# Optimization experiments

Measured on AMD Instinct MI355X. Metric: run time of the kernel, lower is better.

The kernel has to match this reference:

```python
import jax, jax.numpy as jnp
import numpy as np

B, H, S = 128, 256, 19
K0, D0 = 512, 32
K1, D1 = 512, 64
K2, D2 = 512, 64


def _conv(x, w, b):
    # 3x3 SAME conv, NCHW / OIHW
    y = jax.lax.conv_general_dilated(x, w, (1, 1), 'SAME',
                                     dimension_numbers=('NCHW', 'OIHW', 'NCHW'))
    return y + b[None, :, None, None]


def _bn(x, g, b, eps=1e-5):
    # BatchNorm2d in training mode: batch statistics over (N, H, W)
    m = x.mean((0, 2, 3), keepdims=True)
    v = x.var((0, 2, 3), keepdims=True)
    return g[None, :, None, None] * (x - m) * jax.lax.rsqrt(v + eps) + b[None, :, None, None]


def _vq(lat, E):
    # cdist^2 -> argmin -> gather, with straight-through gradient copy
    shp = lat.shape
    d = E.shape[1]
    lp = lat.reshape(-1, d)                                   # row-major flatten, as torch .view
    dist = (lp * lp).sum(-1, keepdims=True) + (E * E).sum(-1) - 2.0 * (lp @ E.T)
    k = jnp.argmin(dist, axis=-1)
    zd = E[k]
    zg = lp + jax.lax.stop_gradient(zd - lp)
    return k.reshape(shp[0], -1), zd.reshape(shp), zg.reshape(shp)


def setup_inputs() -> dict:
    key = jax.random.key(0)
    ks = iter(jax.random.split(key, 64))
    def rn(shape, s=0.02):
        return (s * jax.random.normal(next(ks), shape)).astype(jnp.float32)
    inp = {
        'observations': jax.random.normal(next(ks), (B, 18, S, S), jnp.float32),
        'hierarchy_usages': jax.random.uniform(next(ks), (B, 2), jnp.float32),
        'h0_conv_w': rn((H, 18, 3, 3), 0.05), 'h0_conv_b': jnp.zeros((H,)),
        'h0_bn_g': jnp.ones((H,)), 'h0_bn_b': jnp.zeros((H,)),
        'rb_c1_w': rn((3, H, H, 3, 3)), 'rb_c1_b': jnp.zeros((3, H)),
        'rb_bn1_g': jnp.ones((3, H)), 'rb_bn1_b': jnp.zeros((3, H)),
        'rb_c2_w': rn((3, H, H, 3, 3)), 'rb_c2_b': jnp.zeros((3, H)),
        'rb_bn2_g': jnp.ones((3, H)), 'rb_bn2_b': jnp.zeros((3, H)),
        'h0_conv2_w': rn((32, H, 3, 3)), 'h0_conv2_b': jnp.zeros((32,)),
        'h0_bn2_g': jnp.ones((32,)), 'h0_bn2_b': jnp.zeros((32,)),
        'E0': rn((K0, D0)), 'E1': rn((K1, D1)), 'E2': rn((K2, D2)),
        'h1_fc_w': rn((D0 * S * S, 256)), 'h1_fc_b': jnp.zeros((256,)),
        'h1_fc2_w': rn((256, D1 * 8)), 'h1_fc2_b': jnp.zeros((D1 * 8,)),
        'h2_fc_w': rn((D1 * 8, 128)), 'h2_fc_b': jnp.zeros((128,)),
        'h2_fc2_w': rn((128, D2 * 8)), 'h2_fc2_b': jnp.zeros((D2 * 8,)),
        'h2_fc3_w': rn((D2 * 8, 128)), 'h2_fc3_b': jnp.zeros((128,)),
        'h2_fc4_w': rn((128, D1 * 8)), 'h2_fc4_b': jnp.zeros((D1 * 8,)),
        'h1_fc3_w': rn((D1 * 8, 256)), 'h1_fc3_b': jnp.zeros((256,)),
        'h1_fc4_w': rn((256, D0 * S * S)), 'h1_fc4_b': jnp.zeros((D0 * S * S,)),
        'policy_w': rn((32 * S * S, 362)), 'policy_b': jnp.zeros((362,)),
        'value_w': rn((32 * S * S, 1)), 'value_b': jnp.zeros((1,)),
    }
    return inp


def _forward(observations, hierarchy_usages, h0_conv_w, h0_conv_b, h0_bn_g, h0_bn_b,
             rb_c1_w, rb_c1_b, rb_bn1_g, rb_bn1_b, rb_c2_w, rb_c2_b, rb_bn2_g, rb_bn2_b,
             h0_conv2_w, h0_conv2_b, h0_bn2_g, h0_bn2_b, E0, E1, E2,
             h1_fc_w, h1_fc_b, h1_fc2_w, h1_fc2_b, h2_fc_w, h2_fc_b, h2_fc2_w, h2_fc2_b,
             h2_fc3_w, h2_fc3_b, h2_fc4_w, h2_fc4_b, h1_fc3_w, h1_fc3_b, h1_fc4_w, h1_fc4_b,
             policy_w, policy_b, value_w, value_b):
    n = observations.shape[0]
    x = jax.nn.relu(_bn(_conv(observations, h0_conv_w, h0_conv_b), h0_bn_g, h0_bn_b))
    for i in range(3):
        xi = x
        x = jax.nn.relu(_bn(_conv(x, rb_c1_w[i], rb_c1_b[i]), rb_bn1_g[i], rb_bn1_b[i]))
        x = _bn(_conv(x, rb_c2_w[i], rb_c2_b[i]), rb_bn2_g[i], rb_bn2_b[i])
        x = jax.nn.relu(xi + x)
    x = jnp.tanh(_bn(_conv(x, h0_conv2_w, h0_conv2_b), h0_bn2_g, h0_bn2_b))  # [B,32,19,19]
    ze0 = x
    k0, zq0, zql0 = _vq(x, E0)
    em0 = jnp.broadcast_to(E0.mean(0)[None, :, None, None], (n, E0.shape[1], S, S))
    x = jax.lax.stop_gradient(x).reshape(-1, 32 * S * S)
    x = jax.nn.relu(x @ h1_fc_w + h1_fc_b)
    x = jnp.tanh(x @ h1_fc2_w + h1_fc2_b).reshape(-1, E1.shape[1], 8)
    ze1 = x
    k1, zq1, zql1 = _vq(x, E1)
    em1 = jnp.broadcast_to(E1.mean(0)[None, :, None], (n, E1.shape[1], 8))
    x = jax.lax.stop_gradient(x).reshape(-1, E1.shape[1] * 8)
    x = jax.nn.relu(x @ h2_fc_w + h2_fc_b)
    x = jnp.tanh(x @ h2_fc2_w + h2_fc2_b).reshape(-1, E2.shape[1], 8)
    ze2 = x
    k2, zq2, zql2 = _vq(x, E2)
    em2 = jnp.broadcast_to(E2.mean(0)[None, :, None], (n, E2.shape[1], 8))
    # top-down decoder path
    x = zql2.reshape(-1, E2.shape[1] * 8)
    x = jax.nn.relu(x @ h2_fc3_w + h2_fc3_b)
    x = jnp.tanh(x @ h2_fc4_w + h2_fc4_b).reshape(-1, E1.shape[1], 8)
    u1 = hierarchy_usages[:, 1][:, None, None]
    x = u1 * zql1 + (1.0 - u1) * x
    x = x.reshape(-1, E1.shape[1] * 8)
    x = jax.nn.relu(x @ h1_fc3_w + h1_fc3_b)
    x = jnp.tanh(x @ h1_fc4_w + h1_fc4_b).reshape(-1, E0.shape[1], S, S)
    u0 = hierarchy_usages[:, 0][:, None, None, None]
    x = u0 * zql0 + (1.0 - u0) * x
    x = x.reshape(-1, 32 * S * S)
    policy = x @ policy_w + policy_b
    value = jnp.tanh(x @ value_w + value_b)
    return (policy, value, ze0, ze1, ze2, zq0, zq1, zq2, k0, k1, k2,
            zql0, zql1, zql2, em0, em1, em2)


def reference(observations, hierarchy_usages, h0_conv_w, h0_conv_b, h0_bn_g, h0_bn_b,
              rb_c1_w, rb_c1_b, rb_bn1_g, rb_bn1_b, rb_c2_w, rb_c2_b, rb_bn2_g, rb_bn2_b,
              h0_conv2_w, h0_conv2_b, h0_bn2_g, h0_bn2_b, E0, E1, E2,
              h1_fc_w, h1_fc_b, h1_fc2_w, h1_fc2_b, h2_fc_w, h2_fc_b, h2_fc2_w, h2_fc2_b,
              h2_fc3_w, h2_fc3_b, h2_fc4_w, h2_fc4_b, h1_fc3_w, h1_fc3_b, h1_fc4_w, h1_fc4_b,
              policy_w, policy_b, value_w, value_b):
    return _forward(observations, hierarchy_usages, h0_conv_w, h0_conv_b, h0_bn_g, h0_bn_b,
                    rb_c1_w, rb_c1_b, rb_bn1_g, rb_bn1_b, rb_c2_w, rb_c2_b, rb_bn2_g, rb_bn2_b,
                    h0_conv2_w, h0_conv2_b, h0_bn2_g, h0_bn2_b, E0, E1, E2,
                    h1_fc_w, h1_fc_b, h1_fc2_w, h1_fc2_b, h2_fc_w, h2_fc_b, h2_fc2_w, h2_fc2_b,
                    h2_fc3_w, h2_fc3_b, h2_fc4_w, h2_fc4_b, h1_fc3_w, h1_fc3_b, h1_fc4_w, h1_fc4_b,
                    policy_w, policy_b, value_w, value_b)
```

## Files before the change

kernel.cpp:

```cpp
#include <hip/hip_runtime.h>
#include <hip/hip_bf16.h>

typedef long long i64;
typedef __attribute__((ext_vector_type(8))) short bf16x8;
typedef __attribute__((ext_vector_type(4))) float f32x4;

static constexpr i64 OUT_POLICY = 0;
static constexpr i64 OUT_VALUE  = 46336;
static constexpr i64 OUT_ZE0    = 46464;
static constexpr i64 OUT_ZE1    = 1525120;
static constexpr i64 OUT_ZE2    = 1590656;
static constexpr i64 OUT_ZQ0    = 1656192;
static constexpr i64 OUT_ZQ1    = 3134848;
static constexpr i64 OUT_ZQ2    = 3200384;
static constexpr i64 OUT_K0     = 3265920;
static constexpr i64 OUT_K1     = 3312128;
static constexpr i64 OUT_K2     = 3313152;
static constexpr i64 OUT_ZQL0   = 3314176;
static constexpr i64 OUT_ZQL1   = 4792832;
static constexpr i64 OUT_ZQL2   = 4858368;
static constexpr i64 OUT_EM0    = 4923904;
static constexpr i64 OUT_EM1    = 6402560;
static constexpr i64 OUT_EM2    = 6468096;
static constexpr i64 OUT_TOTAL  = 6533632;
// ... 11 lines not shown
}

__global__ void wtr_k(const float* __restrict__ w, float* __restrict__ wt,
                      int COUT, int CIN)
{
    int total = COUT * CIN * 9;
    for (int idx = blockIdx.x * blockDim.x + threadIdx.x; idx < total;
         idx += gridDim.x * blockDim.x) {
        int co = idx / (CIN * 9);
        int r  = idx - co * CIN * 9;
        int ci = r / 9;
        int tap = r - ci * 9;
        wt[((i64)tap * CIN + ci) * COUT + co] = w[idx];
    }
}

__global__ void wtr4_k(const float* __restrict__ w, short* __restrict__ wt4,
                       int CIN, int COUT)
{
    int NC = CIN / 32;
    int total = NC * 9 * 2 * 8192;
    for (int idx = blockIdx.x * blockDim.x + threadIdx.x; idx < total;
         idx += gridDim.x * blockDim.x) {
        int tile = idx >> 13;
        int pos  = idx & 8191;
        int row   = pos >> 6;
        int sslot = (pos >> 3) & 7;
        int r     = pos & 7;
        int slot  = sslot ^ (row & 7);
        int k2    = slot * 8 + r;
        int ct = tile & 1;
        int s  = tile >> 1;
        int c  = s / 9, t = s - c * 9;
        int co = ct * 128 + row;
        int ci = c * 32 + (k2 & 31);
        short outv = 0;
        if (co < COUT) {
            float v = w[((i64)co * CIN + ci) * 9 + t];
            float hf;
            short hs = bf16_hi(v, &hf);
            outv = (k2 < 32) ? hs : bf16_of(v - hf);
        }
        wt4[idx] = outv;
    }
}

template<int CIN>
__global__ __launch_bounds__(256)
void convmfma_k(const float* __restrict__ X, const short* __restrict__ WT4,
                float* __restrict__ Y, int coutT)
{
    constexpr int NC = CIN / 32;
    constexpr int NS = NC * 9;
    __shared__ short At[2][8192];
    __shared__ short Bt[2][8192];
    const int tid  = threadIdx.x;
    const int lane = tid & 63;
    const int w    = tid >> 6;
    const int wco  = (w & 1) * 64;
    const int wsp  = (w >> 1) * 64;
    const int col0 = blockIdx.x * 128;
    const int ct   = blockIdx.y;
    const int co0  = ct * 128;

    const int spS = tid & 127;
    const int cig = tid >> 7;
    const int colS = col0 + spS;
    const int nS = colS / 361;
    const int sS = colS - nS * 361;
    const int yS = sS / 19, xS = sS - yS * 19;
    const float* Xb = X + (i64)nS * CIN * 361 + sS;

    float xv[16];

#define A_ISSUE(BUF, S)                                                         \
    {                                                                           \
        const short* gp0 = WT4 + ((i64)((S) * 2 + ct) << 13) + (w << 11) + (lane << 3); \
        short* lp0 = &At[BUF][(w << 11)];                                       \
        __builtin_amdgcn_global_load_lds(gp0,        lp0,        16, 0, 0);     \
        __builtin_amdgcn_global_load_lds(gp0 + 512,  lp0 + 512,  16, 0, 0);     \
        __builtin_amdgcn_global_load_lds(gp0 + 1024, lp0 + 1024, 16, 0, 0);     \
        __builtin_amdgcn_global_load_lds(gp0 + 1536, lp0 + 1536, 16, 0, 0);     \
    }

#define B_LOAD(S)                                                               \
    {                                                                           \
        const int c_ = (S) / 9, t_ = (S) - c_ * 9;                              \
        const int ky_ = t_ / 3, kx_ = t_ - ky_ * 3;                             \
        const bool v_ = (yS + ky_ >= 1) & (yS + ky_ <= 19) &                    \
                        (xS + kx_ >= 1) & (xS + kx_ <= 19);                     \
        const float* xp_ = Xb + (i64)(c_ * 32 + cig * 16) * 361                 \
                              + (ky_ - 1) * 19 + (kx_ - 1);                     \
        _Pragma("unroll")                                                       \
        for (int j = 0; j < 16; j++) xv[j] = v_ ? xp_[(i64)j * 361] : 0.f;      \
    }

#define B_WRITE(BUF)                                                            \
    {                                                                           \
        bf16x8 h0, h1, l0, l1;                                                  \
        _Pragma("unroll")                                                       \
        for (int j = 0; j < 8; j++) {                                           \
            float hf;                                                           \
            short hs = bf16_hi(xv[j], &hf);                                     \
            h0[j] = hs; l0[j] = bf16_of(xv[j] - hf);                            \
        }                                                                       \
        _Pragma("unroll")                                                       \
        for (int j = 0; j < 8; j++) {                                           \
            float hf;                                                           \
            short hs = bf16_hi(xv[8 + j], &hf);                                 \
            h1[j] = hs; l1[j] = bf16_of(xv[8 + j] - hf);                        \
        }                                                                       \
        short* bp = &Bt[BUF][spS << 6];                                         \
        const int sw = spS & 7;                                                 \
        *(bf16x8*)(bp + (((cig * 2 + 0) ^ sw) << 3)) = h0;                      \
        *(bf16x8*)(bp + (((cig * 2 + 1) ^ sw) << 3)) = h1;                      \
        *(bf16x8*)(bp + (((4 + cig * 2 + 0) ^ sw) << 3)) = l0;                  \
        *(bf16x8*)(bp + (((4 + cig * 2 + 1) ^ sw) << 3)) = l1;                  \
    }

    f32x4 acc[4][4];
#pragma unroll
    for (int i = 0; i < 4; i++)
#pragma unroll
        for (int j = 0; j < 4; j++) acc[i][j] = (f32x4){0.f, 0.f, 0.f, 0.f};

    A_ISSUE(0, 0)
    B_LOAD(0)
    B_WRITE(0)
    int cur = 0;
    for (int s = 0; s < NS; s++) {
        __syncthreads();
        if (s + 1 < NS) { A_ISSUE(cur ^ 1, s + 1) B_LOAD(s + 1) }
        {
            bf16x8 bfr[2][4];
#pragma unroll
            for (int hb = 0; hb < 2; hb++)
#pragma unroll
                for (int fb = 0; fb < 4; fb++) {
                    int row = wsp + fb * 16 + (lane & 15);
                    int slot = hb * 4 + (lane >> 4);
                    bfr[hb][fb] = *(const bf16x8*)&Bt[cur][(row << 6) + (((slot ^ (row & 7))) << 3)];
                }
#pragma unroll
            for (int ha = 0; ha < 2; ha++)
#pragma unroll
                for (int fa = 0; fa < 4; fa++) {
                    int row = wco + fa * 16 + (lane & 15);
                    int slot = ha * 4 + (lane >> 4);
                    bf16x8 af = *(const bf16x8*)&At[cur][(row << 6) + (((slot ^ (row & 7))) << 3)];
#pragma unroll
                    for (int hb = 0; hb < 2; hb++)
#pragma unroll
                        for (int fb = 0; fb < 4; fb++)
                            acc[fa][fb] = __builtin_amdgcn_mfma_f32_16x16x32_bf16(
                                af, bfr[hb][fb], acc[fa][fb], 0, 0, 0);
                }
        }
        if (s + 1 < NS) B_WRITE(cur ^ 1)
        cur ^= 1;
    }
#undef A_ISSUE
#undef B_LOAD
#undef B_WRITE

#pragma unroll
    for (int fb = 0; fb < 4; fb++) {
        int col = col0 + wsp + fb * 16 + (lane & 15);
        int nT = col / 361, sT = col - nT * 361;
        float* yp = Y + ((i64)nT * coutT + co0 + wco) * 361 + sT;
#pragma unroll
        for (int fa = 0; fa < 4; fa++)
#pragma unroll
            for (int r = 0; r < 4; r++) {
                int m = fa * 16 + (lane >> 4) * 4 + r;
                if (co0 + wco + m < coutT) yp[(i64)m * 361] = acc[fa][fb][r];
            }
    }
}

template<int CIN>
__global__ __launch_bounds__(256)
void convgemm_k(const float* __restrict__ X, const float* __restrict__ wt,
                float* __restrict__ Y, int wtW, int coW0, int coutT)
{
    constexpr int NCB = (CIN + 15) / 16;
    constexpr int NS  = 9 * NCB;
    __shared__ float Ws[2][16][128];
    __shared__ float Bs[2][16][128];
    const int tid  = threadIdx.x;
    const int col0 = blockIdx.x * 128;
    const int co0  = blockIdx.y * 128;
    const int tn = tid & 15;
    const int tm = (tid >> 4) & 15;
    const int kkS  = tid >> 5;
    const int cS0  = (tid & 31) * 4;

    int y_[4], x_[4];
    const float* Xb[4];
#pragma unroll
    for (int j = 0; j < 4; j++) {
        int colj = col0 + cS0 + j;
        int nj = colj / 361;
        int sj = colj - nj * 361;
        y_[j] = sj / 19;
        x_[j] = sj - y_[j] * 19;
        Xb[j] = X + ((i64)nj * CIN) * 361 + sj;
    }

    float4 wA, wB, bA, bB;

#define STAGE(S)                                                               \
    {                                                                          \
        const int tap_ = (S) / NCB, cb_ = ((S) % NCB) * 16;                    \
        const int ky_ = tap_ / 3, kx_ = tap_ - ky_ * 3;                        \
        const int doff_ = (ky_ - 1) * 19 + (kx_ - 1);                          \
        const int ci0_ = cb_ + kkS, ci1_ = ci0_ + 8;                           \
// ... 53 lines not shown
                    acc[wi][bj] = fmaf(wv[wi], bv[bj], acc[wi][bj]);
        }
        if (s + 1 < NS) WRITE(cur ^ 1)
        cur ^= 1;
    }
#undef STAGE
#undef WRITE

#pragma unroll
    for (int bj = 0; bj < 8; bj++) {
        int lc = (bj < 4) ? (tn * 4 + bj) : (64 + tn * 4 + bj - 4);
        int colT = col0 + lc;
        int nT = colT / 361;
        int sT = colT - nT * 361;
        float* yp = Y + ((i64)nT * coutT + co0) * 361 + sT;
#pragma unroll
        for (int wi = 0; wi < 8; wi++) {
            int co = (wi < 4) ? (tm * 4 + wi) : (64 + tm * 4 + wi - 4);
            if (co0 + co < coutT) yp[(i64)co * 361] = acc[wi][bj];
        }
    }
}

__global__ __launch_bounds__(256)
void bnstats_k(const float* __restrict__ x, const float* __restrict__ g,
               const float* __restrict__ b, float* __restrict__ scale,
               float* __restrict__ shift, int C)
{
    const int c = blockIdx.x;
    float s = 0.f, s2 = 0.f;
    for (int n = 0; n < 128; n++) {
        const float* p = x + ((i64)n * C + c) * 361;
        for (int i = threadIdx.x; i < 361; i += 256) {
            float v = p[i]; s += v; s2 += v * v;
        }
    }
    __shared__ float rs[4], rq[4];
    for (int o = 32; o > 0; o >>= 1) { s += __shfl_down(s, o); s2 += __shfl_down(s2, o); }
    int lane = threadIdx.x & 63, wid = threadIdx.x >> 6;
    if (lane == 0) { rs[wid] = s; rq[wid] = s2; }
    __syncthreads();
    if (threadIdx.x == 0) {
        float S = rs[0] + rs[1] + rs[2] + rs[3];
        float Q = rq[0] + rq[1] + rq[2] + rq[3];
        const float inv = 1.f / 46208.f;
        float m  = S * inv;
        float var = Q * inv - m * m;
        float sc = g[c] * rsqrtf(var + 1e-5f);
        scale[c] = sc;
        shift[c] = b[c] - m * sc;
    }
}

__global__ void bn_relu_k(float* __restrict__ x, const float* __restrict__ scale,
                          const float* __restrict__ shift, int C, int total)
{
    for (int i = blockIdx.x * blockDim.x + threadIdx.x; i < total; i += gridDim.x * blockDim.x) {
        int c = (i / 361) % C;
        float v = fmaf(x[i], scale[c], shift[c]);
        x[i] = v > 0.f ? v : 0.f;
    }
}

__global__ void bn_add_relu_full_k(float* __restrict__ xa, const float* __restrict__ xc,
                                   const float* __restrict__ scale, const float* __restrict__ shift,
                                   int C, int total)
{
    for (int i = blockIdx.x * blockDim.x + threadIdx.x; i < total; i += gridDim.x * blockDim.x) {
        int c = (i / 361) % C;
        float v = xa[i] + fmaf(xc[i], scale[c], shift[c]);
        xa[i] = v > 0.f ? v : 0.f;
    }
}

__global__ void bn_add_relu_slice_k(float* __restrict__ xa, const float* __restrict__ xc,
                                    const float* __restrict__ scale, const float* __restrict__ shift,
                                    int cbase, int total)
{
    for (int i = blockIdx.x * blockDim.x + threadIdx.x; i < total; i += gridDim.x * blockDim.x) {
        int s = i % 361;
        int t = i / 361;
        int ch = t % 64;
        int n = t / 64;
        i64 ai = ((i64)n * 256 + cbase + ch) * 361 + s;
        float v = xa[ai] + fmaf(xc[i], scale[ch], shift[ch]);
        xa[ai] = v > 0.f ? v : 0.f;
    }
}

__global__ void bn_tanh_ws_k(const float* __restrict__ x, const float* __restrict__ scale,
                             const float* __restrict__ shift, float* __restrict__ zf, int total)
{
    for (int i = blockIdx.x * blockDim.x + threadIdx.x; i < total; i += gridDim.x * blockDim.x) {
        int c = (i / 361) & 31;
        zf[i] = tanhf(fmaf(x[i], scale[c], shift[c]));
    }
}

__global__ void prep_k(const float* __restrict__ E0, const float* __restrict__ E1,
                       const float* __restrict__ E2,
                       float* __restrict__ ee0, float* __restrict__ ee1, float* __restrict__ ee2,
                       float* __restrict__ cm0, float* __restrict__ cm1, float* __restrict__ cm2)
{
    int t = threadIdx.x;
    if (blockIdx.x == 0) {
        float s = 0.f; const float* e = E0 + (i64)t * 32;
        for (int d = 0; d < 32; d++) s += e[d] * e[d];
        ee0[t] = s;
    } else if (blockIdx.x == 1) {
        float s = 0.f; const float* e = E1 + (i64)t * 64;
        for (int d = 0; d < 64; d++) s += e[d] * e[d];
        ee1[t] = s;
    } else if (blockIdx.x == 2) {
        float s = 0.f; const float* e = E2 + (i64)t * 64;
        for (int d = 0; d < 64; d++) s += e[d] * e[d];
        ee2[t] = s;
    } else {
        if (t < 32) {
            float s = 0.f; for (int k = 0; k < 512; k++) s += E0[k * 32 + t];
            cm0[t] = s * (1.f / 512.f);
        } else if (t >= 64 && t < 128) {
            int d = t - 64; float s = 0.f; for (int k = 0; k < 512; k++) s += E1[k * 64 + d];
            cm1[d] = s * (1.f / 512.f);
        } else if (t >= 128 && t < 192) {
            int d = t - 128; float s = 0.f; for (int k = 0; k < 512; k++) s += E2[k * 64 + d];
            cm2[d] = s * (1.f / 512.f);
        }
    }
}

__global__ __launch_bounds__(256)
void vq0_k(const float* __restrict__ z, const float* __restrict__ E,
           const float* __restrict__ ee, float* __restrict__ zqf, int* __restrict__ ki)
{
    __shared__ float Es[256 * 32];
    int row = blockIdx.x * 256 + threadIdx.x;
    const bool live = row < 46208;
    const float* zp = z + (i64)(live ? row : 0) * 32;
    float zv[32]; float zz = 0.f;
// ... 100 lines not shown
        int m = tm * 8 + i;
#pragma unroll
        for (int j = 0; j < 4; j++) {
            int n = n0 + tn * 4 + j;
            if (n < N) part[((i64)ks * 128 + m) * N + n] = acc[i][j];
        }
    }
}

__global__ void combine_k(const float* __restrict__ part, const float* __restrict__ bias,
                          float* __restrict__ of, int MN, int N, int ksplit, int act)
{
    for (int i = blockIdx.x * blockDim.x + threadIdx.x; i < MN; i += gridDim.x * blockDim.x) {
        float s = 0.f;
        for (int t = 0; t < ksplit; t++) s += part[(i64)t * MN + i];
        s += bias[i % N];
        if (act == 1) s = s > 0.f ? s : 0.f;
        else if (act == 2) s = tanhf(s);
        of[i] = s;
    }
}

__global__ void blend_k(const float* __restrict__ q, const float* __restrict__ d,
                        const float* __restrict__ hu, int col, float* __restrict__ o,
                        int per_b, int total)
{
    for (int i = blockIdx.x * blockDim.x + threadIdx.x; i < total; i += gridDim.x * blockDim.x) {
        float u = hu[(i / per_b) * 2 + col];
        o[i] = u * q[i] + (1.f - u) * d[i];
    }
}

__global__ __launch_bounds__(256)
void value_k(const float* __restrict__ x, const float* __restrict__ w,
             const float* __restrict__ b, float* __restrict__ valf)
{
    int m = blockIdx.x;
    float s = 0.f;
    const float* xp = x + (i64)m * 11552;
    for (int k = threadIdx.x; k < 11552; k += 256) s = fmaf(xp[k], w[k], s);
    for (int o = 32; o > 0; o >>= 1) s += __shfl_down(s, o);
    __shared__ float r[4];
    int lane = threadIdx.x & 63, wid = threadIdx.x >> 6;
    if (lane == 0) r[wid] = s;
    __syncthreads();
    if (threadIdx.x == 0)
        valf[m] = tanhf(r[0] + r[1] + r[2] + r[3] + b[0]);
}

__global__ void emit_f32_k(const float* __restrict__ src, float* __restrict__ out, i64 off, int n)
{
    for (int i = blockIdx.x * blockDim.x + threadIdx.x; i < n; i += gridDim.x * blockDim.x)
        out[off + i] = src[i];
}

__global__ void emit_k_k(const int* __restrict__ ki, float* __restrict__ out, i64 off, int n)
{
    for (int i = blockIdx.x * blockDim.x + threadIdx.x; i < n; i += gridDim.x * blockDim.x)
        out[off + i] = (float)ki[i];
}

__global__ void emit_em_k(const float* __restrict__ cm, float* __restrict__ out, i64 off,
                          int D, int SPL, int total)
{
    for (int i = blockIdx.x * blockDim.x + threadIdx.x; i < total; i += gridDim.x * blockDim.x) {
        int c = (i / SPL) % D;
        out[off + i] = cm[c];
    }
}

__global__ void marker_k(float* __restrict__ out, int code)
{
    if (threadIdx.x < 64) out[threadIdx.x] = 3000.f + 100.f * code;
}

__global__ void sentinel_k(float* __restrict__ out)
{
    if (threadIdx.x < 128) out[OUT_VALUE + threadIdx.x] = 2000.0f;
}

extern "C" void kernel_launch(void* const* d_in, const int* in_sizes, int n_in,
                              void* d_out, int out_size, void* d_ws, size_t ws_size,
                              hipStream_t stream)
{
    float* out = (float*)d_out;

    int bad = -1;
    if (out_size != (int)OUT_TOTAL) bad = 0;
    else if (n_in != 41) bad = 1;
    else if (in_sizes[0] != 128 * 18 * 361) bad = 2;
    else if (in_sizes[21] != 11552 * 256) bad = 3;
    if (bad >= 0) { marker_k<<<1, 64, 0, stream>>>(out, bad); return; }

    const float* obs   = (const float*)d_in[0];
    const float* hier  = (const float*)d_in[1];
    const float* c0w   = (const float*)d_in[2];
    const float* bn0g  = (const float*)d_in[4];
    const float* bn0b  = (const float*)d_in[5];
    const float* rb1w  = (const float*)d_in[6];
    const float* rbn1g = (const float*)d_in[8];
    const float* rbn1b = (const float*)d_in[9];
    const float* rb2w  = (const float*)d_in[10];
    const float* rbn2g = (const float*)d_in[12];
    const float* rbn2b = (const float*)d_in[13];
    const float* c2w   = (const float*)d_in[14];
    const float* bn2g  = (const float*)d_in[16];
// ... 12 lines not shown
    const float* polw  = (const float*)d_in[37]; const float* polb  = (const float*)d_in[38];
    const float* valw  = (const float*)d_in[39]; const float* valb  = (const float*)d_in[40];

    float* wsf = (float*)d_ws;

    const size_t NEED_A = (size_t)36732928 * 4;
    const size_t NEED_C = (size_t)27860992 * 4;
    if (ws_size < NEED_C) {
        sentinel_k<<<1, 128, 0, stream>>>(out);
        return;
    }
    const bool fullC = (ws_size >= NEED_A);

    float* scale = wsf + 0;        float* shift = wsf + 256;
    float* ee0 = wsf + 512;        float* ee1 = wsf + 1024;   float* ee2 = wsf + 1536;
    float* cm0 = wsf + 2048;       float* cm1 = wsf + 2112;   float* cm2 = wsf + 2176;
    int*   k0i = (int*)(wsf + 4096);
    int*   k1i = (int*)(wsf + 50304);
    int*   k2i = (int*)(wsf + 51328);
    float* h1a  = wsf + 53248;
    float* ze1f = wsf + 86016;
    float* zq1f = wsf + 151552;
    float* h2a  = wsf + 217088;
    float* ze2f = wsf + 233472;
    float* zq2f = wsf + 299008;
    float* h2b  = wsf + 364544;
    float* decf = wsf + 380928;
    float* x1f  = wsf + 446464;
    float* h1b  = wsf + 512000;
    float* polf = wsf + 544768;
    float* valf = wsf + 591104;

    float* A    = wsf + 655360;
    float* B    = wsf + 12484608;
    float* C    = wsf + 24313856;
    float* WT   = fullC ? (wsf + 36143104) : (wsf + 27271168);
    float* ze0f = A;
    float* zq0f = wsf + 655360 + 1572864;
    float* dec0 = wsf + 655360 + 3145728;
    float* xf   = wsf + 655360 + 4718592;
    float* part = B;

    short* WT4 = (short*)d_out;

    const int TOT256 = 128 * 256 * 361;
    const int TOT32  = 128 * 32 * 361;
    const int TOT64  = 128 * 64 * 361;

    prep_k<<<4, 512, 0, stream>>>(E0, E1, E2, ee0, ee1, ee2, cm0, cm1, cm2);

    wtr_k<<<64, 256, 0, stream>>>(c0w, WT, 256, 18);
    convgemm_k<18><<<dim3(361, 2), 256, 0, stream>>>(obs, WT, A, 256, 0, 256);
    bnstats_k<<<256, 256, 0, stream>>>(A, bn0g, bn0b, scale, shift, 256);
    bn_relu_k<<<1024, 256, 0, stream>>>(A, scale, shift, 256, TOT256);

    for (int i = 0; i < 3; i++) {
        if (fullC) {
            wtr4_k<<<1024, 256, 0, stream>>>(rb1w + (i64)i * 589824, WT4, 256, 256);
            convmfma_k<256><<<dim3(361, 2), 256, 0, stream>>>(A, WT4, B, 256);
        } else {
            wtr_k<<<576, 256, 0, stream>>>(rb1w + (i64)i * 589824, WT, 256, 256);
            convgemm_k<256><<<dim3(361, 2), 256, 0, stream>>>(A, WT, B, 256, 0, 256);
        }
        bnstats_k<<<256, 256, 0, stream>>>(B, rbn1g + i * 256, rbn1b + i * 256, scale, shift, 256);
        bn_relu_k<<<1024, 256, 0, stream>>>(B, scale, shift, 256, TOT256);
        if (fullC) {
            wtr4_k<<<1024, 256, 0, stream>>>(rb2w + (i64)i * 589824, WT4, 256, 256);
            convmfma_k<256><<<dim3(361, 2), 256, 0, stream>>>(B, WT4, C, 256);
            bnstats_k<<<256, 256, 0, stream>>>(C, rbn2g + i * 256, rbn2b + i * 256, scale, shift, 256);
            bn_add_relu_full_k<<<1024, 256, 0, stream>>>(A, C, scale, shift, 256, TOT256);
        } else {
            wtr_k<<<576, 256, 0, stream>>>(rb2w + (i64)i * 589824, WT, 256, 256);
            for (int c = 0; c < 4; c++) {
                convgemm_k<256><<<dim3(361, 1), 256, 0, stream>>>(B, WT, C, 256, c * 64, 64);
                bnstats_k<<<64, 256, 0, stream>>>(C, rbn2g + i * 256 + c * 64,
                                                  rbn2b + i * 256 + c * 64, scale, shift, 64);
                bn_add_relu_slice_k<<<1024, 256, 0, stream>>>(A, C, scale, shift, c * 64, TOT64);
            }
        }
    }

    if (fullC) {
        wtr4_k<<<1024, 256, 0, stream>>>(c2w, WT4, 256, 32);
        convmfma_k<256><<<dim3(361, 1), 256, 0, stream>>>(A, WT4, C, 32);
    } else {
        wtr_k<<<72, 256, 0, stream>>>(c2w, WT, 32, 256);
        convgemm_k<256><<<dim3(361, 1), 256, 0, stream>>>(A, WT, C, 32, 0, 32);
    }
    bnstats_k<<<32, 256, 0, stream>>>(C, bn2g, bn2b, scale, shift, 32);
    bn_tanh_ws_k<<<1024, 256, 0, stream>>>(C, scale, shift, ze0f, TOT32);

    vq0_k<<<181, 256, 0, stream>>>(ze0f, E0, ee0, zq0f, k0i);

    gemm_part_k<<<dim3(4, 32), 256, 0, stream>>>(ze0f, fc1w, part, 11552, 256, 361);
    combine_k<<<128, 256, 0, stream>>>(part, fc1b, h1a, 128 * 256, 256, 32, 1);
    gemm_part_k<<<dim3(8, 4), 256, 0, stream>>>(h1a, fc2w, part, 256, 512, 64);
    combine_k<<<256, 256, 0, stream>>>(part, fc2b, ze1f, 128 * 512, 512, 4, 2);
    vq64_k<<<4, 256, 0, stream>>>(ze1f, E1, ee1, zq1f, k1i);

    gemm_part_k<<<dim3(2, 8), 256, 0, stream>>>(ze1f, h2fw, part, 512, 128, 64);
    combine_k<<<64, 256, 0, stream>>>(part, h2fb, h2a, 128 * 128, 128, 8, 1);
    gemm_part_k<<<dim3(8, 2), 256, 0, stream>>>(h2a, h2f2w, part, 128, 512, 64);
    combine_k<<<256, 256, 0, stream>>>(part, h2f2b, ze2f, 128 * 512, 512, 2, 2);
    vq64_k<<<4, 256, 0, stream>>>(ze2f, E2, ee2, zq2f, k2i);

    gemm_part_k<<<dim3(2, 8), 256, 0, stream>>>(zq2f, h2f3w, part, 512, 128, 64);
    combine_k<<<64, 256, 0, stream>>>(part, h2f3b, h2b, 128 * 128, 128, 8, 1);
    gemm_part_k<<<dim3(8, 2), 256, 0, stream>>>(h2b, h2f4w, part, 128, 512, 64);
    combine_k<<<256, 256, 0, stream>>>(part, h2f4b, decf, 128 * 512, 512, 2, 2);
    blend_k<<<256, 256, 0, stream>>>(zq1f, decf, hier, 1, x1f, 512, 65536);

    gemm_part_k<<<dim3(4, 8), 256, 0, stream>>>(x1f, h1f3w, part, 512, 256, 64);
    combine_k<<<128, 256, 0, stream>>>(part, h1f3b, h1b, 128 * 256, 256, 8, 1);
    gemm_part_k<<<dim3(181, 2), 256, 0, stream>>>(h1b, h1f4w, part, 256, 11552, 128);
    combine_k<<<1024, 256, 0, stream>>>(part, h1f4b, dec0, TOT32, 11552, 2, 2);
    blend_k<<<1024, 256, 0, stream>>>(zq0f, dec0, hier, 0, xf, 11552, TOT32);

    gemm_part_k<<<dim3(6, 16), 256, 0, stream>>>(xf, polw, part, 11552, 362, 722);
    combine_k<<<256, 256, 0, stream>>>(part, polb, polf, 128 * 362, 362, 16, 0);
    value_k<<<128, 256, 0, stream>>>(xf, valw, valb, valf);

    emit_f32_k<<<128, 256, 0, stream>>>(polf, out, OUT_POLICY, 46336);
    emit_f32_k<<<1, 128, 0, stream>>>(valf, out, OUT_VALUE, 128);
    emit_f32_k<<<1024, 256, 0, stream>>>(ze0f, out, OUT_ZE0, TOT32);
    emit_f32_k<<<256, 256, 0, stream>>>(ze1f, out, OUT_ZE1, 65536);
    emit_f32_k<<<256, 256, 0, stream>>>(ze2f, out, OUT_ZE2, 65536);
    emit_f32_k<<<1024, 256, 0, stream>>>(zq0f, out, OUT_ZQ0, TOT32);
    emit_f32_k<<<256, 256, 0, stream>>>(zq1f, out, OUT_ZQ1, 65536);
    emit_f32_k<<<256, 256, 0, stream>>>(zq2f, out, OUT_ZQ2, 65536);
    emit_k_k<<<181, 256, 0, stream>>>(k0i, out, OUT_K0, 46208);
    emit_k_k<<<4, 256, 0, stream>>>(k1i, out, OUT_K1, 1024);
    emit_k_k<<<4, 256, 0, stream>>>(k2i, out, OUT_K2, 1024);
    emit_f32_k<<<1024, 256, 0, stream>>>(zq0f, out, OUT_ZQL0, TOT32);
    emit_f32_k<<<256, 256, 0, stream>>>(zq1f, out, OUT_ZQL1, 65536);
    emit_f32_k<<<256, 256, 0, stream>>>(zq2f, out, OUT_ZQL2, 65536);
    emit_em_k<<<1024, 256, 0, stream>>>(cm0, out, OUT_EM0, 32, 361, TOT32);
    emit_em_k<<<256, 256, 0, stream>>>(cm1, out, OUT_EM1, 64, 8, 65536);
    emit_em_k<<<256, 256, 0, stream>>>(cm2, out, OUT_EM2, 64, 8, 65536);
}
```

Baseline: 3.365 ms.

## Deepen conv MFMA pipeline, vectorize BN kernels, merge fallback conv, fuse emits

The MFMA conv main loop now prefetches the activation registers two stages ahead using two register sets, and replaces __syncthreads with hand-written waitcnt plus barrier that leaves outstanding vector loads in flight. This aims to hide global load latency behind the MFMA work. The BN+ReLU and BN+add+ReLU elementwise kernels switch to float4 accesses, and the non-fullC fallback runs a single full conv instead of four 64-channel slices. The duplicated zq/zql output copies are merged into one kernel that writes both. The manual vmcnt(16) count depends on how many loads the compiler actually issues and is fragile, and the extra register set adds register pressure.

```diff
diff --git a/kernel.cpp b/kernel.cpp
--- a/kernel.cpp
+++ b/kernel.cpp
@@ -106,7 +106,10 @@
     const int yS = sS / 19, xS = sS - yS * 19;
     const float* Xb = X + (i64)nS * CIN * 361 + sS;
 
-    float xv[16];
+    float xvP[16], xvQ[16];
+
+#define BAR16 asm volatile("s_waitcnt vmcnt(16) lgkmcnt(0)\n\ts_barrier" ::: "memory")
+#define BAR0  asm volatile("s_waitcnt vmcnt(0) lgkmcnt(0)\n\ts_barrier" ::: "memory")
 
 #define A_ISSUE(BUF, S)                                                         \
     {                                                                           \
@@ -118,7 +121,7 @@
         __builtin_amdgcn_global_load_lds(gp0 + 1536, lp0 + 1536, 16, 0, 0);     \
     }
 
-#define B_LOAD(S)                                                               \
+#define B_LOAD(S, XV)                                                           \
     {                                                                           \
         const int c_ = (S) / 9, t_ = (S) - c_ * 9;                              \
         const int ky_ = t_ / 3, kx_ = t_ - ky_ * 3;                             \
@@ -127,23 +130,23 @@
         const float* xp_ = Xb + (i64)(c_ * 32 + cig * 16) * 361                 \
                               + (ky_ - 1) * 19 + (kx_ - 1);                     \
         _Pragma("unroll")                                                       \
-        for (int j = 0; j < 16; j++) xv[j] = v_ ? xp_[(i64)j * 361] : 0.f;      \
-    }
-
-#define B_WRITE(BUF)                                                            \
+        for (int j = 0; j < 16; j++) XV[j] = v_ ? xp_[(i64)j * 361] : 0.f;      \
+    }
+
+#define B_WRITE(BUF, XV)                                                        \
     {                                                                           \
         bf16x8 h0, h1, l0, l1;                                                  \
         _Pragma("unroll")                                                       \
         for (int j = 0; j < 8; j++) {                                           \
             float hf;                                                           \
-            short hs = bf16_hi(xv[j], &hf);                                     \
-            h0[j] = hs; l0[j] = bf16_of(xv[j] - hf);                            \
+            short hs = bf16_hi(XV[j], &hf);                                     \
+            h0[j] = hs; l0[j] = bf16_of(XV[j] - hf);                            \
         }                                                                       \
         _Pragma("unroll")                                                       \
         for (int j = 0; j < 8; j++) {                                           \
             float hf;                                                           \
-            short hs = bf16_hi(xv[8 + j], &hf);                                 \
-            h1[j] = hs; l1[j] = bf16_of(xv[8 + j] - hf);                        \
+            short hs = bf16_hi(XV[8 + j], &hf);                                 \
+            h1[j] = hs; l1[j] = bf16_of(XV[8 + j] - hf);                        \
         }                                                                       \
         short* bp = &Bt[BUF][spS << 6];                                         \
         const int sw = spS & 7;                                                 \
@@ -153,50 +156,65 @@
         *(bf16x8*)(bp + (((4 + cig * 2 + 1) ^ sw) << 3)) = l1;                  \
     }
 
+#define COMPUTE(CUR)                                                            \
+    {                                                                           \
+        bf16x8 bfr[2][4];                                                       \
+        _Pragma("unroll")                                                       \
+        for (int hb = 0; hb < 2; hb++)                                          \
+            _Pragma("unroll")                                                   \
+            for (int fb = 0; fb < 4; fb++) {                                    \
+                int row = wsp + fb * 16 + (lane & 15);                          \
+                int slot = hb * 4 + (lane >> 4);                                \
+                bfr[hb][fb] = *(const bf16x8*)&Bt[CUR][(row << 6) + (((slot ^ (row & 7))) << 3)]; \
+            }                                                                   \
+        _Pragma("unroll")                                                       \
+        for (int ha = 0; ha < 2; ha++)                                          \
+            _Pragma("unroll")                                                   \
+            for (int fa = 0; fa < 4; fa++) {                                    \
+                int row = wco + fa * 16 + (lane & 15);                          \
+                int slot = ha * 4 + (lane >> 4);                                \
+                bf16x8 af = *(const bf16x8*)&At[CUR][(row << 6) + (((slot ^ (row & 7))) << 3)]; \
+                _Pragma("unroll")                                               \
+                for (int hb = 0; hb < 2; hb++)                                  \
+                    _Pragma("unroll")                                           \
+                    for (int fb = 0; fb < 4; fb++)                              \
+                        acc[fa][fb] = __builtin_amdgcn_mfma_f32_16x16x32_bf16(  \
+                            af, bfr[hb][fb], acc[fa][fb], 0, 0, 0);             \
+            }                                                                   \
+    }
+
+#define ITER(S, XP, XN)                                                         \
+    {                                                                           \
+        if ((S) + 1 < NS) { BAR16; } else { BAR0; }                             \
+        const int cur_ = ((S) & 1);                                             \
+        if ((S) + 1 < NS) A_ISSUE(cur_ ^ 1, (S) + 1)                            \
+        if ((S) + 2 < NS) B_LOAD((S) + 2, XN)                                   \
+        COMPUTE(cur_)                                                           \
+        if ((S) + 1 < NS) B_WRITE(cur_ ^ 1, XP)                                 \
+    }
+
     f32x4 acc[4][4];
 #pragma unroll
     for (int i = 0; i < 4; i++)
 #pragma unroll
         for (int j = 0; j < 4; j++) acc[i][j] = (f32x4){0.f, 0.f, 0.f, 0.f};
 
+    B_LOAD(0, xvP)
+    B_WRITE(0, xvP)
     A_ISSUE(0, 0)
-    B_LOAD(0)
-    B_WRITE(0)
-    int cur = 0;
-    for (int s = 0; s < NS; s++) {
-        __syncthreads();
-        if (s + 1 < NS) { A_ISSUE(cur ^ 1, s + 1) B_LOAD(s + 1) }
-        {
-            bf16x8 bfr[2][4];
-#pragma unroll
-            for (int hb = 0; hb < 2; hb++)
-#pragma unroll
-                for (int fb = 0; fb < 4; fb++) {
-                    int row = wsp + fb * 16 + (lane & 15);
-                    int slot = hb * 4 + (lane >> 4);
-                    bfr[hb][fb] = *(const bf16x8*)&Bt[cur][(row << 6) + (((slot ^ (row & 7))) << 3)];
-                }
-#pragma unroll
-            for (int ha = 0; ha < 2; ha++)
-#pragma unroll
-                for (int fa = 0; fa < 4; fa++) {
-                    int row = wco + fa * 16 + (lane & 15);
-                    int slot = ha * 4 + (lane >> 4);
-                    bf16x8 af = *(const bf16x8*)&At[cur][(row << 6) + (((slot ^ (row & 7))) << 3)];
-#pragma unroll
-                    for (int hb = 0; hb < 2; hb++)
-#pragma unroll
-                        for (int fb = 0; fb < 4; fb++)
-                            acc[fa][fb] = __builtin_amdgcn_mfma_f32_16x16x32_bf16(
-                                af, bfr[hb][fb], acc[fa][fb], 0, 0, 0);
-                }
-        }
-        if (s + 1 < NS) B_WRITE(cur ^ 1)
-        cur ^= 1;
-    }
+    B_LOAD(1, xvP)
+
+    for (int s = 0; s < NS; s += 2) {
+        ITER(s, xvP, xvQ)
+        ITER(s + 1, xvQ, xvP)
+    }
+#undef BAR16
+#undef BAR0
 #undef A_ISSUE
 #undef B_LOAD
 #undef B_WRITE
+#undef COMPUTE
+#undef ITER
 
 #pragma unroll
     for (int fb = 0; fb < 4; fb++) {
@@ -356,39 +374,36 @@
     }
 }
 
-__global__ void bn_relu_k(float* __restrict__ x, const float* __restrict__ scale,
-                          const float* __restrict__ shift, int C, int total)
-{
-    for (int i = blockIdx.x * blockDim.x + threadIdx.x; i < total; i += gridDim.x * blockDim.x) {
-        int c = (i / 361) % C;
-        float v = fmaf(x[i], scale[c], shift[c]);
-        x[i] = v > 0.f ? v : 0.f;
-    }
-}
-
-__global__ void bn_add_relu_full_k(float* __restrict__ xa, const float* __restrict__ xc,
-                                   const float* __restrict__ scale, const float* __restrict__ shift,
-                                   int C, int total)
-{
-    for (int i = blockIdx.x * blockDim.x + threadIdx.x; i < total; i += gridDim.x * blockDim.x) {
-        int c = (i / 361) % C;
-        float v = xa[i] + fmaf(xc[i], scale[c], shift[c]);
-        xa[i] = v > 0.f ? v : 0.f;
-    }
-}
-
-__global__ void bn_add_relu_slice_k(float* __restrict__ xa, const float* __restrict__ xc,
-                                    const float* __restrict__ scale, const float* __restrict__ shift,
-                                    int cbase, int total)
-{
-    for (int i = blockIdx.x * blockDim.x + threadIdx.x; i < total; i += gridDim.x * blockDim.x) {
-        int s = i % 361;
-        int t = i / 361;
-        int ch = t % 64;
-        int n = t / 64;
-        i64 ai = ((i64)n * 256 + cbase + ch) * 361 + s;
-        float v = xa[ai] + fmaf(xc[i], scale[ch], shift[ch]);
-        xa[ai] = v > 0.f ? v : 0.f;
+__global__ void bn_relu4_k(float4* __restrict__ x, const float* __restrict__ scale,
+                           const float* __restrict__ shift, int C, int total4)
+{
+    for (int i = blockIdx.x * blockDim.x + threadIdx.x; i < total4; i += gridDim.x * blockDim.x) {
+        float4 v = x[i];
+        int e = i * 4;
+        int c0 = (e / 361) % C, c1 = ((e + 1) / 361) % C;
+        int c2 = ((e + 2) / 361) % C, c3 = ((e + 3) / 361) % C;
+        v.x = fmaf(v.x, scale[c0], shift[c0]); v.x = v.x > 0.f ? v.x : 0.f;
+        v.y = fmaf(v.y, scale[c1], shift[c1]); v.y = v.y > 0.f ? v.y : 0.f;
+        v.z = fmaf(v.z, scale[c2], shift[c2]); v.z = v.z > 0.f ? v.z : 0.f;
+        v.w = fmaf(v.w, scale[c3], shift[c3]); v.w = v.w > 0.f ? v.w : 0.f;
+        x[i] = v;
+    }
+}
+
+__global__ void bn_add_relu4_k(float4* __restrict__ xa, const float4* __restrict__ xc,
+                               const float* __restrict__ scale, const float* __restrict__ shift,
+                               int C, int total4)
+{
+    for (int i = blockIdx.x * blockDim.x + threadIdx.x; i < total4; i += gridDim.x * blockDim.x) {
+        float4 a = xa[i], c = xc[i];
+        int e = i * 4;
+        int c0 = (e / 361) % C, c1 = ((e + 1) / 361) % C;
+        int c2 = ((e + 2) / 361) % C, c3 = ((e + 3) / 361) % C;
+        a.x += fmaf(c.x, scale[c0], shift[c0]); a.x = a.x > 0.f ? a.x : 0.f;
+        a.y += fmaf(c.y, scale[c1], shift[c1]); a.y = a.y > 0.f ? a.y : 0.f;
+        a.z += fmaf(c.z, scale[c2], shift[c2]); a.z = a.z > 0.f ? a.z : 0.f;
+        a.w += fmaf(c.w, scale[c3], shift[c3]); a.w = a.w > 0.f ? a.w : 0.f;
+        xa[i] = a;
     }
 }
 
@@ -595,6 +610,16 @@
 {
     for (int i = blockIdx.x * blockDim.x + threadIdx.x; i < n; i += gridDim.x * blockDim.x)
         out[off + i] = src[i];
+}
+
+__global__ void emit_dup_k(const float* __restrict__ src, float* __restrict__ out,
+                           i64 off1, i64 off2, int n)
+{
+    for (int i = blockIdx.x * blockDim.x + threadIdx.x; i < n; i += gridDim.x * blockDim.x) {
+        float v = src[i];
+        out[off1 + i] = v;
+        out[off2 + i] = v;
+    }
 }
 
 __global__ void emit_k_k(const int* __restrict__ ki, float* __restrict__ out, i64 off, int n)
@@ -713,7 +738,7 @@
     wtr_k<<<64, 256, 0, stream>>>(c0w, WT, 256, 18);
     convgemm_k<18><<<dim3(361, 2), 256, 0, stream>>>(obs, WT, A, 256, 0, 256);
     bnstats_k<<<256, 256, 0, stream>>>(A, bn0g, bn0b, scale, shift, 256);
-    bn_relu_k<<<1024, 256, 0, stream>>>(A, scale, shift, 256, TOT256);
+    bn_relu4_k<<<1024, 256, 0, stream>>>((float4*)A, scale, shift, 256, TOT256 / 4);
 
     for (int i = 0; i < 3; i++) {
         if (fullC) {
@@ -724,20 +749,17 @@
             convgemm_k<256><<<dim3(361, 2), 256, 0, stream>>>(A, WT, B, 256, 0, 256);
         }
         bnstats_k<<<256, 256, 0, stream>>>(B, rbn1g + i * 256, rbn1b + i * 256, scale, shift, 256);
-        bn_relu_k<<<1024, 256, 0, stream>>>(B, scale, shift, 256, TOT256);
+        bn_relu4_k<<<1024, 256, 0, stream>>>((float4*)B, scale, shift, 256, TOT256 / 4);
         if (fullC) {
             wtr4_k<<<1024, 256, 0, stream>>>(rb2w + (i64)i * 589824, WT4, 256, 256);
             convmfma_k<256><<<dim3(361, 2), 256, 0, stream>>>(B, WT4, C, 256);
             bnstats_k<<<256, 256, 0, stream>>>(C, rbn2g + i * 256, rbn2b + i * 256, scale, shift, 256);
-            bn_add_relu_full_k<<<1024, 256, 0, stream>>>(A, C, scale, shift, 256, TOT256);
+            bn_add_relu4_k<<<1024, 256, 0, stream>>>((float4*)A, (const float4*)C, scale, shift, 256, TOT256 / 4);
         } else {
             wtr_k<<<576, 256, 0, stream>>>(rb2w + (i64)i * 589824, WT, 256, 256);
-            for (int c = 0; c < 4; c++) {
-                convgemm_k<256><<<dim3(361, 1), 256, 0, stream>>>(B, WT, C, 256, c * 64, 64);
-                bnstats_k<<<64, 256, 0, stream>>>(C, rbn2g + i * 256 + c * 64,
-                                                  rbn2b + i * 256 + c * 64, scale, shift, 64);
-                bn_add_relu_slice_k<<<1024, 256, 0, stream>>>(A, C, scale, shift, c * 64, TOT64);
-            }
+            convgemm_k<256><<<dim3(361, 2), 256, 0, stream>>>(B, WT, C, 256, 0, 256);
+            bnstats_k<<<256, 256, 0, stream>>>(C, rbn2g + i * 256, rbn2b + i * 256, scale, shift, 256);
+            bn_add_relu4_k<<<1024, 256, 0, stream>>>((float4*)A, (const float4*)C, scale, shift, 256, TOT256 / 4);
         }
     }
 
@@ -786,15 +808,12 @@
     emit_f32_k<<<1024, 256, 0, stream>>>(ze0f, out, OUT_ZE0, TOT32);
     emit_f32_k<<<256, 256, 0, stream>>>(ze1f, out, OUT_ZE1, 65536);
     emit_f32_k<<<256, 256, 0, stream>>>(ze2f, out, OUT_ZE2, 65536);
-    emit_f32_k<<<1024, 256, 0, stream>>>(zq0f, out, OUT_ZQ0, TOT32);
-    emit_f32_k<<<256, 256, 0, stream>>>(zq1f, out, OUT_ZQ1, 65536);
-    emit_f32_k<<<256, 256, 0, stream>>>(zq2f, out, OUT_ZQ2, 65536);
+    emit_dup_k<<<1024, 256, 0, stream>>>(zq0f, out, OUT_ZQ0, OUT_ZQL0, TOT32);
+    emit_dup_k<<<256, 256, 0, stream>>>(zq1f, out, OUT_ZQ1, OUT_ZQL1, 65536);
+    emit_dup_k<<<256, 256, 0, stream>>>(zq2f, out, OUT_ZQ2, OUT_ZQL2, 65536);
     emit_k_k<<<181, 256, 0, stream>>>(k0i, out, OUT_K0, 46208);
     emit_k_k<<<4, 256, 0, stream>>>(k1i, out, OUT_K1, 1024);
     emit_k_k<<<4, 256, 0, stream>>>(k2i, out, OUT_K2, 1024);
-    emit_f32_k<<<1024, 256, 0, stream>>>(zq0f, out, OUT_ZQL0, TOT32);
-    emit_f32_k<<<256, 256, 0, stream>>>(zq1f, out, OUT_ZQL1, 65536);
-    emit_f32_k<<<256, 256, 0, stream>>>(zq2f, out, OUT_ZQL2, 65536);
     emit_em_k<<<1024, 256, 0, stream>>>(cm0, out, OUT_EM0, 32, 361, TOT32);
     emit_em_k<<<256, 256, 0, stream>>>(cm1, out, OUT_EM1, 64, 8, 65536);
     emit_em_k<<<256, 256, 0, stream>>>(cm2, out, OUT_EM2, 64, 8, 65536);
```

Measured after the change: 3.592 ms. 6.7% more time.

## Load conv weights directly to registers, vectorize BN kernels, merge emits

Applied to the files above, without the earlier changes.

The MFMA conv kernel no longer stages weight tiles through LDS with global_load_lds. Each wave now reads its A fragments straight from global memory into registers every step, which halves shared memory use but puts global latency inside the MFMA loop. The BN/ReLU elementwise kernels are rewritten to use float4 accesses. The fallback residual path now runs one full-width conv instead of four channel-slice launches, and duplicate zq output writes are merged into a single dual-store kernel.

```diff
diff --git a/kernel.cpp b/kernel.cpp
--- a/kernel.cpp
+++ b/kernel.cpp
@@ -87,7 +87,6 @@
 {
     constexpr int NC = CIN / 32;
     constexpr int NS = NC * 9;
-    __shared__ short At[2][8192];
     __shared__ short Bt[2][8192];
     const int tid  = threadIdx.x;
     const int lane = tid & 63;
@@ -107,16 +106,6 @@
     const float* Xb = X + (i64)nS * CIN * 361 + sS;
 
     float xv[16];
-
-#define A_ISSUE(BUF, S)                                                         \
-    {                                                                           \
-        const short* gp0 = WT4 + ((i64)((S) * 2 + ct) << 13) + (w << 11) + (lane << 3); \
-        short* lp0 = &At[BUF][(w << 11)];                                       \
-        __builtin_amdgcn_global_load_lds(gp0,        lp0,        16, 0, 0);     \
-        __builtin_amdgcn_global_load_lds(gp0 + 512,  lp0 + 512,  16, 0, 0);     \
-        __builtin_amdgcn_global_load_lds(gp0 + 1024, lp0 + 1024, 16, 0, 0);     \
-        __builtin_amdgcn_global_load_lds(gp0 + 1536, lp0 + 1536, 16, 0, 0);     \
-    }
 
 #define B_LOAD(S)                                                               \
     {                                                                           \
@@ -159,14 +148,23 @@
 #pragma unroll
         for (int j = 0; j < 4; j++) acc[i][j] = (f32x4){0.f, 0.f, 0.f, 0.f};
 
-    A_ISSUE(0, 0)
     B_LOAD(0)
     B_WRITE(0)
     int cur = 0;
     for (int s = 0; s < NS; s++) {
         __syncthreads();
-        if (s + 1 < NS) { A_ISSUE(cur ^ 1, s + 1) B_LOAD(s + 1) }
+        if (s + 1 < NS) B_LOAD(s + 1)
         {
+            const short* tb = WT4 + ((i64)(s * 2 + ct) << 13);
+            bf16x8 afr[2][4];
+#pragma unroll
+            for (int ha = 0; ha < 2; ha++)
+#pragma unroll
+                for (int fa = 0; fa < 4; fa++) {
+                    int row = wco + fa * 16 + (lane & 15);
+                    int slot = ha * 4 + (lane >> 4);
+                    afr[ha][fa] = *(const bf16x8*)(tb + (row << 6) + (((slot ^ (row & 7))) << 3));
+                }
             bf16x8 bfr[2][4];
 #pragma unroll
             for (int hb = 0; hb < 2; hb++)
@@ -180,9 +178,7 @@
             for (int ha = 0; ha < 2; ha++)
 #pragma unroll
                 for (int fa = 0; fa < 4; fa++) {
-                    int row = wco + fa * 16 + (lane & 15);
-                    int slot = ha * 4 + (lane >> 4);
-                    bf16x8 af = *(const bf16x8*)&At[cur][(row << 6) + (((slot ^ (row & 7))) << 3)];
+                    bf16x8 af = afr[ha][fa];
 #pragma unroll
                     for (int hb = 0; hb < 2; hb++)
 #pragma unroll
@@ -194,7 +190,6 @@
         if (s + 1 < NS) B_WRITE(cur ^ 1)
         cur ^= 1;
     }
-#undef A_ISSUE
 #undef B_LOAD
 #undef B_WRITE
 
@@ -356,39 +351,36 @@
     }
 }
 
-__global__ void bn_relu_k(float* __restrict__ x, const float* __restrict__ scale,
-                          const float* __restrict__ shift, int C, int total)
-{
-    for (int i = blockIdx.x * blockDim.x + threadIdx.x; i < total; i += gridDim.x * blockDim.x) {
-        int c = (i / 361) % C;
-        float v = fmaf(x[i], scale[c], shift[c]);
-        x[i] = v > 0.f ? v : 0.f;
-    }
-}
-
-__global__ void bn_add_relu_full_k(float* __restrict__ xa, const float* __restrict__ xc,
-                                   const float* __restrict__ scale, const float* __restrict__ shift,
-                                   int C, int total)
-{
-    for (int i = blockIdx.x * blockDim.x + threadIdx.x; i < total; i += gridDim.x * blockDim.x) {
-        int c = (i / 361) % C;
-        float v = xa[i] + fmaf(xc[i], scale[c], shift[c]);
-        xa[i] = v > 0.f ? v : 0.f;
-    }
-}
-
-__global__ void bn_add_relu_slice_k(float* __restrict__ xa, const float* __restrict__ xc,
-                                    const float* __restrict__ scale, const float* __restrict__ shift,
-                                    int cbase, int total)
-{
-    for (int i = blockIdx.x * blockDim.x + threadIdx.x; i < total; i += gridDim.x * blockDim.x) {
-        int s = i % 361;
-        int t = i / 361;
-        int ch = t % 64;
-        int n = t / 64;
-        i64 ai = ((i64)n * 256 + cbase + ch) * 361 + s;
-        float v = xa[ai] + fmaf(xc[i], scale[ch], shift[ch]);
-        xa[ai] = v > 0.f ? v : 0.f;
+__global__ void bn_relu4_k(float4* __restrict__ x, const float* __restrict__ scale,
+                           const float* __restrict__ shift, int C, int total4)
+{
+    for (int i = blockIdx.x * blockDim.x + threadIdx.x; i < total4; i += gridDim.x * blockDim.x) {
+        float4 v = x[i];
+        int e = i * 4;
+        int c0 = (e / 361) % C, c1 = ((e + 1) / 361) % C;
+        int c2 = ((e + 2) / 361) % C, c3 = ((e + 3) / 361) % C;
+        v.x = fmaf(v.x, scale[c0], shift[c0]); v.x = v.x > 0.f ? v.x : 0.f;
+        v.y = fmaf(v.y, scale[c1], shift[c1]); v.y = v.y > 0.f ? v.y : 0.f;
+        v.z = fmaf(v.z, scale[c2], shift[c2]); v.z = v.z > 0.f ? v.z : 0.f;
+        v.w = fmaf(v.w, scale[c3], shift[c3]); v.w = v.w > 0.f ? v.w : 0.f;
+        x[i] = v;
+    }
+}
+
+__global__ void bn_add_relu4_k(float4* __restrict__ xa, const float4* __restrict__ xc,
+                               const float* __restrict__ scale, const float* __restrict__ shift,
+                               int C, int total4)
+{
+    for (int i = blockIdx.x * blockDim.x + threadIdx.x; i < total4; i += gridDim.x * blockDim.x) {
+        float4 a = xa[i], c = xc[i];
+        int e = i * 4;
+        int c0 = (e / 361) % C, c1 = ((e + 1) / 361) % C;
+        int c2 = ((e + 2) / 361) % C, c3 = ((e + 3) / 361) % C;
+        a.x += fmaf(c.x, scale[c0], shift[c0]); a.x = a.x > 0.f ? a.x : 0.f;
+        a.y += fmaf(c.y, scale[c1], shift[c1]); a.y = a.y > 0.f ? a.y : 0.f;
+        a.z += fmaf(c.z, scale[c2], shift[c2]); a.z = a.z > 0.f ? a.z : 0.f;
+        a.w += fmaf(c.w, scale[c3], shift[c3]); a.w = a.w > 0.f ? a.w : 0.f;
+        xa[i] = a;
     }
 }
 
@@ -595,6 +587,16 @@
 {
     for (int i = blockIdx.x * blockDim.x + threadIdx.x; i < n; i += gridDim.x * blockDim.x)
         out[off + i] = src[i];
+}
+
+__global__ void emit_dup_k(const float* __restrict__ src, float* __restrict__ out,
+                           i64 off1, i64 off2, int n)
+{
+    for (int i = blockIdx.x * blockDim.x + threadIdx.x; i < n; i += gridDim.x * blockDim.x) {
+        float v = src[i];
+        out[off1 + i] = v;
+        out[off2 + i] = v;
+    }
 }
 
 __global__ void emit_k_k(const int* __restrict__ ki, float* __restrict__ out, i64 off, int n)
@@ -713,7 +715,7 @@
     wtr_k<<<64, 256, 0, stream>>>(c0w, WT, 256, 18);
     convgemm_k<18><<<dim3(361, 2), 256, 0, stream>>>(obs, WT, A, 256, 0, 256);
     bnstats_k<<<256, 256, 0, stream>>>(A, bn0g, bn0b, scale, shift, 256);
-    bn_relu_k<<<1024, 256, 0, stream>>>(A, scale, shift, 256, TOT256);
+    bn_relu4_k<<<1024, 256, 0, stream>>>((float4*)A, scale, shift, 256, TOT256 / 4);
 
     for (int i = 0; i < 3; i++) {
         if (fullC) {
@@ -724,20 +726,17 @@
             convgemm_k<256><<<dim3(361, 2), 256, 0, stream>>>(A, WT, B, 256, 0, 256);
         }
         bnstats_k<<<256, 256, 0, stream>>>(B, rbn1g + i * 256, rbn1b + i * 256, scale, shift, 256);
-        bn_relu_k<<<1024, 256, 0, stream>>>(B, scale, shift, 256, TOT256);
+        bn_relu4_k<<<1024, 256, 0, stream>>>((float4*)B, scale, shift, 256, TOT256 / 4);
         if (fullC) {
             wtr4_k<<<1024, 256, 0, stream>>>(rb2w + (i64)i * 589824, WT4, 256, 256);
             convmfma_k<256><<<dim3(361, 2), 256, 0, stream>>>(B, WT4, C, 256);
             bnstats_k<<<256, 256, 0, stream>>>(C, rbn2g + i * 256, rbn2b + i * 256, scale, shift, 256);
-            bn_add_relu_full_k<<<1024, 256, 0, stream>>>(A, C, scale, shift, 256, TOT256);
+            bn_add_relu4_k<<<1024, 256, 0, stream>>>((float4*)A, (const float4*)C, scale, shift, 256, TOT256 / 4);
         } else {
             wtr_k<<<576, 256, 0, stream>>>(rb2w + (i64)i * 589824, WT, 256, 256);
-            for (int c = 0; c < 4; c++) {
-                convgemm_k<256><<<dim3(361, 1), 256, 0, stream>>>(B, WT, C, 256, c * 64, 64);
-                bnstats_k<<<64, 256, 0, stream>>>(C, rbn2g + i * 256 + c * 64,
-                                                  rbn2b + i * 256 + c * 64, scale, shift, 64);
-                bn_add_relu_slice_k<<<1024, 256, 0, stream>>>(A, C, scale, shift, c * 64, TOT64);
-            }
+            convgemm_k<256><<<dim3(361, 2), 256, 0, stream>>>(B, WT, C, 256, 0, 256);
+            bnstats_k<<<256, 256, 0, stream>>>(C, rbn2g + i * 256, rbn2b + i * 256, scale, shift, 256);
+            bn_add_relu4_k<<<1024, 256, 0, stream>>>((float4*)A, (const float4*)C, scale, shift, 256, TOT256 / 4);
         }
     }
 
@@ -786,15 +785,12 @@
     emit_f32_k<<<1024, 256, 0, stream>>>(ze0f, out, OUT_ZE0, TOT32);
     emit_f32_k<<<256, 256, 0, stream>>>(ze1f, out, OUT_ZE1, 65536);
     emit_f32_k<<<256, 256, 0, stream>>>(ze2f, out, OUT_ZE2, 65536);
-    emit_f32_k<<<1024, 256, 0, stream>>>(zq0f, out, OUT_ZQ0, TOT32);
-    emit_f32_k<<<256, 256, 0, stream>>>(zq1f, out, OUT_ZQ1, 65536);
-    emit_f32_k<<<256, 256, 0, stream>>>(zq2f, out, OUT_ZQ2, 65536);
+    emit_dup_k<<<1024, 256, 0, stream>>>(zq0f, out, OUT_ZQ0, OUT_ZQL0, TOT32);
+    emit_dup_k<<<256, 256, 0, stream>>>(zq1f, out, OUT_ZQ1, OUT_ZQL1, 65536);
+    emit_dup_k<<<256, 256, 0, stream>>>(zq2f, out, OUT_ZQ2, OUT_ZQL2, 65536);
     emit_k_k<<<181, 256, 0, stream>>>(k0i, out, OUT_K0, 46208);
     emit_k_k<<<4, 256, 0, stream>>>(k1i, out, OUT_K1, 1024);
     emit_k_k<<<4, 256, 0, stream>>>(k2i, out, OUT_K2, 1024);
-    emit_f32_k<<<1024, 256, 0, stream>>>(zq0f, out, OUT_ZQL0, TOT32);
-    emit_f32_k<<<256, 256, 0, stream>>>(zq1f, out, OUT_ZQL1, 65536);
-    emit_f32_k<<<256, 256, 0, stream>>>(zq2f, out, OUT_ZQL2, 65536);
     emit_em_k<<<1024, 256, 0, stream>>>(cm0, out, OUT_EM0, 32, 361, TOT32);
     emit_em_k<<<256, 256, 0, stream>>>(cm1, out, OUT_EM1, 64, 8, 65536);
     emit_em_k<<<256, 256, 0, stream>>>(cm2, out, OUT_EM2, 64, 8, 65536);
```

Result: no change. 3.344 ms (-0.6%).
